# Optimization experiments

Hardware: AMD Instinct MI355X
Metric: run time of the kernel (lower is better)

## Reference

```python
import jax, jax.numpy as jnp
import numpy as np

NUM_LAYERS = 4
HIDDEN = 32
INPUT = 2
B = 16384
T = 64


def setup_inputs() -> dict:
    key = jax.random.key(0)
    ks = jax.random.split(key, 8)
    s = 1.0 / np.sqrt(HIDDEN)  # PyTorch LSTM default init scale
    return {
        "x": jax.random.normal(ks[0], (B, 3, T), dtype=jnp.float32),
        "W_ih0": jax.random.uniform(ks[1], (4 * HIDDEN, INPUT), minval=-s, maxval=s, dtype=jnp.float32),
        "W_ih": jax.random.uniform(ks[2], (NUM_LAYERS - 1, 4 * HIDDEN, HIDDEN), minval=-s, maxval=s, dtype=jnp.float32),
        "W_hh": jax.random.uniform(ks[3], (NUM_LAYERS, 4 * HIDDEN, HIDDEN), minval=-s, maxval=s, dtype=jnp.float32),
        "b_ih": jax.random.uniform(ks[4], (NUM_LAYERS, 4 * HIDDEN), minval=-s, maxval=s, dtype=jnp.float32),
        "b_hh": jax.random.uniform(ks[5], (NUM_LAYERS, 4 * HIDDEN), minval=-s, maxval=s, dtype=jnp.float32),
        "W_lin": jax.random.uniform(ks[6], (1, HIDDEN), minval=-s, maxval=s, dtype=jnp.float32),
        "b_lin": jax.random.uniform(ks[7], (1,), minval=-s, maxval=s, dtype=jnp.float32),
    }


def _lstm_cell(inp, h, c, Wih, Whh, b):
    # inp: [B, in_dim]; h, c: [B, H]; Wih: [4H, in_dim]; Whh: [4H, H]; b: [4H]
    gates = inp @ Wih.T + h @ Whh.T + b  # [B, 4H]
    i, f, g, o = jnp.split(gates, 4, axis=-1)  # PyTorch gate order: i, f, g, o
    i = jax.nn.sigmoid(i)
    f = jax.nn.sigmoid(f)
    g = jnp.tanh(g)
    o = jax.nn.sigmoid(o)
    c_new = f * c + i * g
    h_new = o * jnp.tanh(c_new)
    return h_new, c_new


def reference(x, W_ih0, W_ih, W_hh, b_ih, b_hh, W_lin, b_lin):
    # x: [B, 3, T]; channel 2 (id) is discarded, as in the original forward.
    feats = x[:, :2, :]                         # [B, 2, T]
    xs = jnp.transpose(feats, (2, 0, 1))        # [T, B, 2]
    bsz = x.shape[0]
    h0 = jnp.zeros((NUM_LAYERS, bsz, HIDDEN), dtype=x.dtype)
    c0 = jnp.zeros((NUM_LAYERS, bsz, HIDDEN), dtype=x.dtype)
    bias = b_ih + b_hh  # [L, 4H]

    def step(carry, xt):
        h, c = carry  # each [L, B, H]
        inp = xt
        hs, cs = [], []
        for l in range(NUM_LAYERS):
            Wih = W_ih0 if l == 0 else W_ih[l - 1]
            h_new, c_new = _lstm_cell(inp, h[l], c[l], Wih, W_hh[l], bias[l])
            hs.append(h_new)
            cs.append(c_new)
            inp = h_new
        return (jnp.stack(hs), jnp.stack(cs)), None

    (h, c), _ = jax.lax.scan(step, (h0, c0), xs)
    # last timestep's top-layer output -> linear -> sigmoid -> squeeze to [B]
    out = jax.nn.sigmoid(h[-1] @ W_lin.T + b_lin)  # [B, 1]
    return out.squeeze(-1)
```

## Files before the change

kernel.cpp:

```cpp
#include <hip/hip_runtime.h>

typedef float  f32x4  __attribute__((ext_vector_type(4)));
typedef float  f32x2  __attribute__((ext_vector_type(2)));
typedef short  bf16x8 __attribute__((ext_vector_type(8)));

#define TWOLOG2E   2.8853900817779268f
#define NLOG2E    -1.4426950408889634f
#define NTWOLOG2E -2.8853900817779268f

__device__ __forceinline__ unsigned short f2b(float f) {
    unsigned int u = __builtin_bit_cast(unsigned int, f);
    u += 0x7fffu + ((u >> 16) & 1u);
    return (unsigned short)(u >> 16);
}
__device__ __forceinline__ float b2f(unsigned short s) {
    unsigned int u = ((unsigned int)s) << 16;
    return __builtin_bit_cast(float, u);
}
__device__ __forceinline__ unsigned int pk2(float lo, float hi) {
#if __has_builtin(__builtin_amdgcn_cvt_pk_bf16_f32)
    typedef __bf16 bf16x2 __attribute__((ext_vector_type(2)));
    bf16x2 p = __builtin_amdgcn_cvt_pk_bf16_f32(lo, hi);
    return __builtin_bit_cast(unsigned int, p);
#else
    return (unsigned int)f2b(lo) | ((unsigned int)f2b(hi) << 16);
#endif
}
__device__ __forceinline__ float frcp(float x) { return __builtin_amdgcn_rcpf(x); }
__device__ __forceinline__ float fex2(float x) { return __builtin_amdgcn_exp2f(x); }

__global__ __launch_bounds__(256, 2)
void lstm_mfma(const float* __restrict__ xg,  const float* __restrict__ Wih0,
               const float* __restrict__ Wih, const float* __restrict__ Whh,
               const float* __restrict__ bih, const float* __restrict__ bhh,
               const float* __restrict__ Wlin,const float* __restrict__ blin,
               float* __restrict__ out) {
    __shared__ short        hb[16 * 1280] __attribute__((aligned(16)));
    __shared__ unsigned int xb[64 * 32];

    const int tid  = threadIdx.x;
    const int wv   = __builtin_amdgcn_readfirstlane(tid >> 6);
    const int lane = tid & 63;
    const int m    = lane & 15;
    const int q    = lane >> 4;
    const int row0 = blockIdx.x * 32;

    for (int i = tid; i < 10240; i += 256) ((unsigned int*)hb)[i] = 0u;

    for (int i = tid; i < 2048; i += 256) {
        int r = i >> 6, t = i & 63;
        float x0 = xg[(size_t)(row0 + r) * 192 + t];
        float x1 = xg[(size_t)(row0 + r) * 192 + 64 + t];
        xb[t * 32 + r] = pk2(x0, x1);
    }

    bf16x8 bfr[8][2];
    float  bv[8];
#pragma unroll
    for (int g = 0; g < 8; ++g) {
        const int   T    = g >> 1;
        const int   rowG = T * 32 + 2 * m + (g & 1);
        const float sc   = (T == 2) ? NTWOLOG2E : NLOG2E;
        bv[g] = (bih[wv * 128 + rowG] + bhh[wv * 128 + rowG]) * sc;
#pragma unroll
        for (int c = 0; c < 2; ++c) {
            const int k0 = c * 32 + q * 8;
            float w[8];
            if (wv == 0) {
                if (c == 0) {
#pragma unroll
                    for (int jj = 0; jj < 8; ++jj) w[jj] = 0.0f;
                    if (q == 0) { w[0] = Wih0[rowG * 2]; w[1] = Wih0[rowG * 2 + 1]; }
                } else {
                    const float* src = Whh + rowG * 32 + (k0 - 32);
#pragma unroll
                    for (int jj = 0; jj < 8; ++jj) w[jj] = src[jj];
                }
            } else {
                const float* src = (c == 0) ? (Wih + (wv - 1) * 4096 + rowG * 32 + k0)
                                            : (Whh + wv * 4096 + rowG * 32 + (k0 - 32));
#pragma unroll
                for (int jj = 0; jj < 8; ++jj) w[jj] = src[jj];
            }
            bf16x8 fr;
#pragma unroll
            for (int jj = 0; jj < 8; ++jj) fr[jj] = (short)f2b(w[jj] * sc);
            bfr[g][c] = fr;
        }
    }

    f32x4 cbq[8];
#pragma unroll
    for (int g = 0; g < 8; ++g) {
        f32x4 c4 = {bv[g], bv[g], bv[g], bv[g]};
        cbq[g] = c4;
    }

    f32x2 cp2[2][4];
#pragma unroll
    for (int tt = 0; tt < 2; ++tt)
#pragma unroll
        for (int r = 0; r < 4; ++r) cp2[tt][r] = (f32x2){0.0f, 0.0f};

    const int aoff = m * 40 + q * 8;
    const int woff = q * 80 + m;

    __syncthreads();

    auto cell_step = [&](int t, const short* pa0, const short* pa1, short* hwr) {
        bf16x8 a0[2], a1[2];
#pragma unroll
        for (int tt = 0; tt < 2; ++tt) {
            if (wv == 0) {
                unsigned int xd = xb[t * 32 + tt * 16 + m];
                union { unsigned int u[4]; bf16x8 v; } au;
                au.u[0] = (q == 0) ? xd : 0u; au.u[1] = 0u; au.u[2] = 0u; au.u[3] = 0u;
                a0[tt] = au.v;
            } else {
                a0[tt] = *(const bf16x8*)(pa0 + aoff + tt * 640);
            }
            a1[tt] = *(const bf16x8*)(pa1 + aoff + tt * 640);
        }
#pragma unroll
        for (int tt = 0; tt < 2; ++tt) {
            f32x4 acc[8];
#pragma unroll
            for (int g = 0; g < 8; ++g) {
                acc[g] = __builtin_amdgcn_mfma_f32_16x16x32_bf16(a0[tt], bfr[g][0], cbq[g], 0, 0, 0);
                acc[g] = __builtin_amdgcn_mfma_f32_16x16x32_bf16(a1[tt], bfr[g][1], acc[g], 0, 0, 0);
            }
            const f32x2 one  = {1.0f, 1.0f};
            const f32x2 c2l  = {TWOLOG2E, TWOLOG2E};
            const f32x2 n2l  = {NTWOLOG2E, NTWOLOG2E};
#pragma unroll
            for (int r = 0; r < 4; ++r) {
                f32x2 ei = {fex2(acc[0][r]), fex2(acc[1][r])};
                f32x2 ef = {fex2(acc[2][r]), fex2(acc[3][r])};
                f32x2 eg = {fex2(acc[4][r]), fex2(acc[5][r])};
                f32x2 eo = {fex2(acc[6][r]), fex2(acc[7][r])};
                f32x2 apf = one + ef;
                f32x2 p1  = (one + ei) * (one + eg);
                f32x2 Dc  = p1 * apf;
                f32x2 R_  = {frcp(Dc.x), frcp(Dc.y)};
                f32x2 egp = __builtin_elementwise_fma(eg, c2l, n2l);
                f32x2 t1  = egp * apf;
                f32x2 t2  = __builtin_elementwise_fma(cp2[tt][r], p1, t1);
                f32x2 cn  = t2 * R_;
                cp2[tt][r] = cn;
                f32x2 ec  = {fex2(cn.x), fex2(cn.y)};
                f32x2 Dh  = (one + eo) * (one + ec);
                f32x2 Rh  = {frcp(Dh.x), frcp(Dh.y)};
                f32x2 hh  = (one - ec) * Rh;
                ((unsigned int*)hwr)[woff + tt * 320 + r * 20] = pk2(hh.x, hh.y);
            }
        }
    };

    for (int S = 0; S < 35; ++S) {
        const int t0 = 2 * (S - wv);
        if (t0 >= 0 && t0 <= 62) {
            const int p  = S & 1;
            const int pb = p ^ 1;
            short*       Lc0 = hb + ((wv * 2 + p ) * 2    ) * 1280;
            short*       Lc1 = Lc0 + 1280;
            const short* Lp1 = hb + ((wv * 2 + pb) * 2 + 1) * 1280;
            const int    lb  = (wv > 0) ? (wv - 1) : 0;
            const short* Dp0 = hb + ((lb * 2 + pb) * 2    ) * 1280;
            const short* Dp1 = Dp0 + 1280;

            cell_step(t0,     Dp0, Lp1, Lc0);
            cell_step(t0 + 1, Dp1, Lc0, Lc1);
        }
        __syncthreads();
    }

    if (tid < 32) {
        const short* h3 = hb + ((3 * 2 + 0) * 2 + 1) * 1280;
        float s = blin[0];
#pragma unroll
        for (int k = 0; k < 32; ++k)
            s += Wlin[k] * b2f((unsigned short)h3[tid * 40 + k]);
        out[row0 + tid] = frcp(1.0f + fex2(s * NLOG2E));
    }
}

extern "C" void kernel_launch(void* const* d_in, const int* in_sizes, int n_in,
                              void* d_out, int out_size, void* d_ws, size_t ws_size,
                              hipStream_t stream) {
    const float* x    = (const float*)d_in[0];
    const float* Wih0 = (const float*)d_in[1];
    const float* Wih  = (const float*)d_in[2];
    const float* Whh  = (const float*)d_in[3];
    const float* bih  = (const float*)d_in[4];
    const float* bhh  = (const float*)d_in[5];
    const float* Wlin = (const float*)d_in[6];
    const float* blin = (const float*)d_in[7];
    float* out = (float*)d_out;

    lstm_mfma<<<512, 256, 0, stream>>>(x, Wih0, Wih, Whh, bih, bhh, Wlin, blin, out);
}
```

Measured before the change: 215.5 us.

## Halve rows per block to 16 and raise occupancy to four blocks per CU

Each block now handles 16 batch rows instead of 32, so the grid doubles to 1024 blocks and shared memory per block halves. The launch bound goes from 2 to 4 blocks per CU, and the bias is added after the MFMA instead of being held in a replicated accumulator, which cuts register use. The aim is more concurrent waves to hide the latency of the serial recurrence chain. In exchange, each wave gets less independent MFMA work per step, since two 16-row tiles no longer interleave.

```diff
diff --git a/kernel.cpp b/kernel.cpp
--- a/kernel.cpp
+++ b/kernel.cpp
@@ -29,29 +29,29 @@
 __device__ __forceinline__ float frcp(float x) { return __builtin_amdgcn_rcpf(x); }
 __device__ __forceinline__ float fex2(float x) { return __builtin_amdgcn_exp2f(x); }
 
-__global__ __launch_bounds__(256, 2)
+__global__ __launch_bounds__(256, 4)
 void lstm_mfma(const float* __restrict__ xg,  const float* __restrict__ Wih0,
                const float* __restrict__ Wih, const float* __restrict__ Whh,
                const float* __restrict__ bih, const float* __restrict__ bhh,
                const float* __restrict__ Wlin,const float* __restrict__ blin,
                float* __restrict__ out) {
-    __shared__ short        hb[16 * 1280] __attribute__((aligned(16)));
-    __shared__ unsigned int xb[64 * 32];
+    __shared__ short        hb[16 * 640] __attribute__((aligned(16)));
+    __shared__ unsigned int xb[64 * 16];
 
     const int tid  = threadIdx.x;
     const int wv   = __builtin_amdgcn_readfirstlane(tid >> 6);
     const int lane = tid & 63;
     const int m    = lane & 15;
     const int q    = lane >> 4;
-    const int row0 = blockIdx.x * 32;
+    const int row0 = blockIdx.x * 16;
 
-    for (int i = tid; i < 10240; i += 256) ((unsigned int*)hb)[i] = 0u;
+    for (int i = tid; i < 5120; i += 256) ((unsigned int*)hb)[i] = 0u;
 
-    for (int i = tid; i < 2048; i += 256) {
+    for (int i = tid; i < 1024; i += 256) {
         int r = i >> 6, t = i & 63;
         float x0 = xg[(size_t)(row0 + r) * 192 + t];
         float x1 = xg[(size_t)(row0 + r) * 192 + 64 + t];
-        xb[t * 32 + r] = pk2(x0, x1);
+        xb[t * 16 + r] = pk2(x0, x1);
     }
 
     bf16x8 bfr[8][2];
@@ -89,18 +89,13 @@
         }
     }
 
-    f32x4 cbq[8];
+    f32x2 bvp[4];
 #pragma unroll
-    for (int g = 0; g < 8; ++g) {
-        f32x4 c4 = {bv[g], bv[g], bv[g], bv[g]};
-        cbq[g] = c4;
-    }
+    for (int T = 0; T < 4; ++T) bvp[T] = (f32x2){bv[2 * T], bv[2 * T + 1]};
 
-    f32x2 cp2[2][4];
+    f32x2 cp2[4];
 #pragma unroll
-    for (int tt = 0; tt < 2; ++tt)
-#pragma unroll
-        for (int r = 0; r < 4; ++r) cp2[tt][r] = (f32x2){0.0f, 0.0f};
+    for (int r = 0; r < 4; ++r) cp2[r] = (f32x2){0.0f, 0.0f};
 
     const int aoff = m * 40 + q * 8;
     const int woff = q * 80 + m;
@@ -108,51 +103,51 @@
     __syncthreads();
 
     auto cell_step = [&](int t, const short* pa0, const short* pa1, short* hwr) {
-        bf16x8 a0[2], a1[2];
+        bf16x8 a0, a1;
+        if (wv == 0) {
+            unsigned int xd = xb[t * 16 + m];
+            union { unsigned int u[4]; bf16x8 v; } au;
+            au.u[0] = (q == 0) ? xd : 0u; au.u[1] = 0u; au.u[2] = 0u; au.u[3] = 0u;
+            a0 = au.v;
+        } else {
+            a0 = *(const bf16x8*)(pa0 + aoff);
+        }
+        a1 = *(const bf16x8*)(pa1 + aoff);
+
+        const f32x4 zq = {0.0f, 0.0f, 0.0f, 0.0f};
+        f32x4 acc[8];
 #pragma unroll
-        for (int tt = 0; tt < 2; ++tt) {
-            if (wv == 0) {
-                unsigned int xd = xb[t * 32 + tt * 16 + m];
-                union { unsigned int u[4]; bf16x8 v; } au;
-                au.u[0] = (q == 0) ? xd : 0u; au.u[1] = 0u; au.u[2] = 0u; au.u[3] = 0u;
-                a0[tt] = au.v;
-            } else {
-                a0[tt] = *(const bf16x8*)(pa0 + aoff + tt * 640);
-            }
-            a1[tt] = *(const bf16x8*)(pa1 + aoff + tt * 640);
+        for (int g = 0; g < 8; ++g) {
+            acc[g] = __builtin_amdgcn_mfma_f32_16x16x32_bf16(a0, bfr[g][0], zq, 0, 0, 0);
+            acc[g] = __builtin_amdgcn_mfma_f32_16x16x32_bf16(a1, bfr[g][1], acc[g], 0, 0, 0);
         }
+        const f32x2 one  = {1.0f, 1.0f};
+        const f32x2 c2l  = {TWOLOG2E, TWOLOG2E};
+        const f32x2 n2l  = {NTWOLOG2E, NTWOLOG2E};
 #pragma unroll
-        for (int tt = 0; tt < 2; ++tt) {
-            f32x4 acc[8];
-#pragma unroll
-            for (int g = 0; g < 8; ++g) {
-                acc[g] = __builtin_amdgcn_mfma_f32_16x16x32_bf16(a0[tt], bfr[g][0], cbq[g], 0, 0, 0);
-                acc[g] = __builtin_amdgcn_mfma_f32_16x16x32_bf16(a1[tt], bfr[g][1], acc[g], 0, 0, 0);
-            }
-            const f32x2 one  = {1.0f, 1.0f};
-            const f32x2 c2l  = {TWOLOG2E, TWOLOG2E};
-            const f32x2 n2l  = {NTWOLOG2E, NTWOLOG2E};
-#pragma unroll
-            for (int r = 0; r < 4; ++r) {
-                f32x2 ei = {fex2(acc[0][r]), fex2(acc[1][r])};
-                f32x2 ef = {fex2(acc[2][r]), fex2(acc[3][r])};
-                f32x2 eg = {fex2(acc[4][r]), fex2(acc[5][r])};
-                f32x2 eo = {fex2(acc[6][r]), fex2(acc[7][r])};
-                f32x2 apf = one + ef;
-                f32x2 p1  = (one + ei) * (one + eg);
-                f32x2 Dc  = p1 * apf;
-                f32x2 R_  = {frcp(Dc.x), frcp(Dc.y)};
-                f32x2 egp = __builtin_elementwise_fma(eg, c2l, n2l);
-                f32x2 t1  = egp * apf;
-                f32x2 t2  = __builtin_elementwise_fma(cp2[tt][r], p1, t1);
-                f32x2 cn  = t2 * R_;
-                cp2[tt][r] = cn;
-                f32x2 ec  = {fex2(cn.x), fex2(cn.y)};
-                f32x2 Dh  = (one + eo) * (one + ec);
-                f32x2 Rh  = {frcp(Dh.x), frcp(Dh.y)};
-                f32x2 hh  = (one - ec) * Rh;
-                ((unsigned int*)hwr)[woff + tt * 320 + r * 20] = pk2(hh.x, hh.y);
-            }
+        for (int r = 0; r < 4; ++r) {
+            f32x2 gi = (f32x2){acc[0][r], acc[1][r]} + bvp[0];
+            f32x2 gf = (f32x2){acc[2][r], acc[3][r]} + bvp[1];
+            f32x2 gg = (f32x2){acc[4][r], acc[5][r]} + bvp[2];
+            f32x2 go = (f32x2){acc[6][r], acc[7][r]} + bvp[3];
+            f32x2 ei = {fex2(gi.x), fex2(gi.y)};
+            f32x2 ef = {fex2(gf.x), fex2(gf.y)};
+            f32x2 eg = {fex2(gg.x), fex2(gg.y)};
+            f32x2 eo = {fex2(go.x), fex2(go.y)};
+            f32x2 apf = one + ef;
+            f32x2 p1  = (one + ei) * (one + eg);
+            f32x2 Dc  = p1 * apf;
+            f32x2 R_  = {frcp(Dc.x), frcp(Dc.y)};
+            f32x2 egp = __builtin_elementwise_fma(eg, c2l, n2l);
+            f32x2 t1  = egp * apf;
+            f32x2 t2  = __builtin_elementwise_fma(cp2[r], p1, t1);
+            f32x2 cn  = t2 * R_;
+            cp2[r] = cn;
+            f32x2 ec  = {fex2(cn.x), fex2(cn.y)};
+            f32x2 Dh  = (one + eo) * (one + ec);
+            f32x2 Rh  = {frcp(Dh.x), frcp(Dh.y)};
+            f32x2 hh  = (one - ec) * Rh;
+            ((unsigned int*)hwr)[woff + r * 20] = pk2(hh.x, hh.y);
         }
     };
 
@@ -161,12 +156,12 @@
         if (t0 >= 0 && t0 <= 62) {
             const int p  = S & 1;
             const int pb = p ^ 1;
-            short*       Lc0 = hb + ((wv * 2 + p ) * 2    ) * 1280;
-            short*       Lc1 = Lc0 + 1280;
-            const short* Lp1 = hb + ((wv * 2 + pb) * 2 + 1) * 1280;
+            short*       Lc0 = hb + ((wv * 2 + p ) * 2    ) * 640;
+            short*       Lc1 = Lc0 + 640;
+            const short* Lp1 = hb + ((wv * 2 + pb) * 2 + 1) * 640;
             const int    lb  = (wv > 0) ? (wv - 1) : 0;
-            const short* Dp0 = hb + ((lb * 2 + pb) * 2    ) * 1280;
-            const short* Dp1 = Dp0 + 1280;
+            const short* Dp0 = hb + ((lb * 2 + pb) * 2    ) * 640;
+            const short* Dp1 = Dp0 + 640;
 
             cell_step(t0,     Dp0, Lp1, Lc0);
             cell_step(t0 + 1, Dp1, Lc0, Lc1);
@@ -174,8 +169,8 @@
         __syncthreads();
     }
 
-    if (tid < 32) {
-        const short* h3 = hb + ((3 * 2 + 0) * 2 + 1) * 1280;
+    if (tid < 16) {
+        const short* h3 = hb + ((3 * 2 + 0) * 2 + 1) * 640;
         float s = blin[0];
 #pragma unroll
         for (int k = 0; k < 32; ++k)
@@ -197,5 +192,5 @@
     const float* blin = (const float*)d_in[7];
     float* out = (float*)d_out;
 
-    lstm_mfma<<<512, 256, 0, stream>>>(x, Wih0, Wih, Whh, bih, bhh, Wlin, blin, out);
+    lstm_mfma<<<1024, 256, 0, stream>>>(x, Wih0, Wih, Whh, bih, bhh, Wlin, blin, out);
 }
```

Measured after the change: 245.4 us. +13.9%, slower.

## Interleave next-timestep input MFMAs with current-step epilogue in LSTM wavefront

Applied to the files above, without the earlier changes.

Splits each two-timestep cell update into separate input-projection and recurrent MFMA phases. The input-side MFMAs for the second timestep are issued between the epilogue tiles of the first timestep, so matrix work overlaps with the exp/rcp epilogue. The bias moves from the MFMA accumulator init into the epilogue as a vector add. This roughly doubles the live accumulator registers, which risks spills or reduced occupancy.

```diff
diff --git a/kernel.cpp b/kernel.cpp
--- a/kernel.cpp
+++ b/kernel.cpp
@@ -89,12 +89,9 @@
         }
     }
 
-    f32x4 cbq[8];
-#pragma unroll
-    for (int g = 0; g < 8; ++g) {
-        f32x4 c4 = {bv[g], bv[g], bv[g], bv[g]};
-        cbq[g] = c4;
-    }
+    f32x2 bvp[4];
+#pragma unroll
+    for (int T = 0; T < 4; ++T) bvp[T] = (f32x2){bv[2 * T], bv[2 * T + 1]};
 
     f32x2 cp2[2][4];
 #pragma unroll
@@ -107,54 +104,59 @@
 
     __syncthreads();
 
-    auto cell_step = [&](int t, const short* pa0, const short* pa1, short* hwr) {
-        bf16x8 a0[2], a1[2];
-#pragma unroll
-        for (int tt = 0; tt < 2; ++tt) {
-            if (wv == 0) {
+    auto load_down = [&](int t, const short* pa, bf16x8* dst) {
+        if (wv == 0) {
+#pragma unroll
+            for (int tt = 0; tt < 2; ++tt) {
                 unsigned int xd = xb[t * 32 + tt * 16 + m];
                 union { unsigned int u[4]; bf16x8 v; } au;
                 au.u[0] = (q == 0) ? xd : 0u; au.u[1] = 0u; au.u[2] = 0u; au.u[3] = 0u;
-                a0[tt] = au.v;
-            } else {
-                a0[tt] = *(const bf16x8*)(pa0 + aoff + tt * 640);
+                dst[tt] = au.v;
             }
-            a1[tt] = *(const bf16x8*)(pa1 + aoff + tt * 640);
-        }
-#pragma unroll
-        for (int tt = 0; tt < 2; ++tt) {
-            f32x4 acc[8];
-#pragma unroll
-            for (int g = 0; g < 8; ++g) {
-                acc[g] = __builtin_amdgcn_mfma_f32_16x16x32_bf16(a0[tt], bfr[g][0], cbq[g], 0, 0, 0);
-                acc[g] = __builtin_amdgcn_mfma_f32_16x16x32_bf16(a1[tt], bfr[g][1], acc[g], 0, 0, 0);
-            }
-            const f32x2 one  = {1.0f, 1.0f};
-            const f32x2 c2l  = {TWOLOG2E, TWOLOG2E};
-            const f32x2 n2l  = {NTWOLOG2E, NTWOLOG2E};
-#pragma unroll
-            for (int r = 0; r < 4; ++r) {
-                f32x2 ei = {fex2(acc[0][r]), fex2(acc[1][r])};
-                f32x2 ef = {fex2(acc[2][r]), fex2(acc[3][r])};
-                f32x2 eg = {fex2(acc[4][r]), fex2(acc[5][r])};
-                f32x2 eo = {fex2(acc[6][r]), fex2(acc[7][r])};
-                f32x2 apf = one + ef;
-                f32x2 p1  = (one + ei) * (one + eg);
-                f32x2 Dc  = p1 * apf;
-                f32x2 R_  = {frcp(Dc.x), frcp(Dc.y)};
-                f32x2 egp = __builtin_elementwise_fma(eg, c2l, n2l);
-                f32x2 t1  = egp * apf;
-                f32x2 t2  = __builtin_elementwise_fma(cp2[tt][r], p1, t1);
-                f32x2 cn  = t2 * R_;
-                cp2[tt][r] = cn;
-                f32x2 ec  = {fex2(cn.x), fex2(cn.y)};
-                f32x2 Dh  = (one + eo) * (one + ec);
-                f32x2 Rh  = {frcp(Dh.x), frcp(Dh.y)};
-                f32x2 hh  = (one - ec) * Rh;
-                ((unsigned int*)hwr)[woff + tt * 320 + r * 20] = pk2(hh.x, hh.y);
-            }
+        } else {
+#pragma unroll
+            for (int tt = 0; tt < 2; ++tt)
+                dst[tt] = *(const bf16x8*)(pa + aoff + tt * 640);
         }
     };
+    auto load_rec = [&](const short* pa, bf16x8* dst) {
+#pragma unroll
+        for (int tt = 0; tt < 2; ++tt)
+            dst[tt] = *(const bf16x8*)(pa + aoff + tt * 640);
+    };
+
+    auto epi_tile = [&](const f32x4* a8, f32x2* cpr, short* hwr, int tt) {
+        const f32x2 one = {1.0f, 1.0f};
+        const f32x2 c2l = {TWOLOG2E, TWOLOG2E};
+        const f32x2 n2l = {NTWOLOG2E, NTWOLOG2E};
+#pragma unroll
+        for (int r = 0; r < 4; ++r) {
+            f32x2 gi = (f32x2){a8[0][r], a8[1][r]} + bvp[0];
+            f32x2 gf = (f32x2){a8[2][r], a8[3][r]} + bvp[1];
+            f32x2 gg = (f32x2){a8[4][r], a8[5][r]} + bvp[2];
+            f32x2 go = (f32x2){a8[6][r], a8[7][r]} + bvp[3];
+            f32x2 ei = {fex2(gi.x), fex2(gi.y)};
+            f32x2 ef = {fex2(gf.x), fex2(gf.y)};
+            f32x2 eg = {fex2(gg.x), fex2(gg.y)};
+            f32x2 eo = {fex2(go.x), fex2(go.y)};
+            f32x2 apf = one + ef;
+            f32x2 p1  = (one + ei) * (one + eg);
+            f32x2 Dc  = p1 * apf;
+            f32x2 R_  = {frcp(Dc.x), frcp(Dc.y)};
+            f32x2 egp = __builtin_elementwise_fma(eg, c2l, n2l);
+            f32x2 t1  = egp * apf;
+            f32x2 t2  = __builtin_elementwise_fma(cpr[r], p1, t1);
+            f32x2 cn  = t2 * R_;
+            cpr[r] = cn;
+            f32x2 ec  = {fex2(cn.x), fex2(cn.y)};
+            f32x2 Dh  = (one + eo) * (one + ec);
+            f32x2 Rh  = {frcp(Dh.x), frcp(Dh.y)};
+            f32x2 hh  = (one - ec) * Rh;
+            ((unsigned int*)hwr)[woff + tt * 320 + r * 20] = pk2(hh.x, hh.y);
+        }
+    };
+
+    const f32x4 zq = {0.0f, 0.0f, 0.0f, 0.0f};
 
     for (int S = 0; S < 35; ++S) {
         const int t0 = 2 * (S - wv);
@@ -168,8 +170,37 @@
             const short* Dp0 = hb + ((lb * 2 + pb) * 2    ) * 1280;
             const short* Dp1 = Dp0 + 1280;
 
-            cell_step(t0,     Dp0, Lp1, Lc0);
-            cell_step(t0 + 1, Dp1, Lc0, Lc1);
+            bf16x8 a0d[2], a0r[2], a1d[2];
+            load_down(t0,     Dp0, a0d);
+            load_rec (Lp1,         a0r);
+            load_down(t0 + 1, Dp1, a1d);
+
+            f32x4 acc0[2][8], acc1[2][8];
+#pragma unroll
+            for (int tt = 0; tt < 2; ++tt)
+#pragma unroll
+                for (int g = 0; g < 8; ++g) {
+                    acc0[tt][g] = __builtin_amdgcn_mfma_f32_16x16x32_bf16(a0d[tt], bfr[g][0], zq, 0, 0, 0);
+                    acc0[tt][g] = __builtin_amdgcn_mfma_f32_16x16x32_bf16(a0r[tt], bfr[g][1], acc0[tt][g], 0, 0, 0);
+                }
+
+            epi_tile(acc0[0], cp2[0], Lc0, 0);
+#pragma unroll
+            for (int tt = 0; tt < 2; ++tt)
+#pragma unroll
+                for (int g = 0; g < 8; ++g)
+                    acc1[tt][g] = __builtin_amdgcn_mfma_f32_16x16x32_bf16(a1d[tt], bfr[g][0], zq, 0, 0, 0);
+            epi_tile(acc0[1], cp2[1], Lc0, 1);
+
+            bf16x8 a1r[2];
+            load_rec(Lc0, a1r);
+#pragma unroll
+            for (int tt = 0; tt < 2; ++tt)
+#pragma unroll
+                for (int g = 0; g < 8; ++g)
+                    acc1[tt][g] = __builtin_amdgcn_mfma_f32_16x16x32_bf16(a1r[tt], bfr[g][1], acc1[tt][g], 0, 0, 0);
+            epi_tile(acc1[0], cp2[0], Lc1, 0);
+            epi_tile(acc1[1], cp2[1], Lc1, 1);
         }
         __syncthreads();
     }
```

New measurement: 231.6 us. +7.5%, slower.

## Transpose MFMA operands so LSTM hidden state stays in registers

Applied to the files above, without the earlier changes.

Swaps the MFMA operand roles so the weights become the A operand and the hidden state becomes the B operand, with gate rows permuted so that each lane's accumulator outputs line up directly with the next step's B-operand layout. The recurrent hidden state is kept in registers (hreg) rather than re-read from LDS, and LDS writes become one 16-byte vector store per lane instead of scattered 4-byte stores. This removes the same-layer LDS read and the LDS zero-init, at the cost of more involved index permutations for weights, biases and the final linear readout.

```diff
diff --git a/kernel.cpp b/kernel.cpp
--- a/kernel.cpp
+++ b/kernel.cpp
@@ -35,7 +35,7 @@
                const float* __restrict__ bih, const float* __restrict__ bhh,
                const float* __restrict__ Wlin,const float* __restrict__ blin,
                float* __restrict__ out) {
-    __shared__ short        hb[16 * 1280] __attribute__((aligned(16)));
+    __shared__ unsigned int hb[16 * 512] __attribute__((aligned(16)));
     __shared__ unsigned int xb[64 * 32];
 
     const int tid  = threadIdx.x;
@@ -45,8 +45,6 @@
     const int q    = lane >> 4;
     const int row0 = blockIdx.x * 32;
 
-    for (int i = tid; i < 10240; i += 256) ((unsigned int*)hb)[i] = 0u;
-
     for (int i = tid; i < 2048; i += 256) {
         int r = i >> 6, t = i & 63;
         float x0 = xg[(size_t)(row0 + r) * 192 + t];
@@ -54,105 +52,116 @@
         xb[t * 32 + r] = pk2(x0, x1);
     }
 
-    bf16x8 bfr[8][2];
-    float  bv[8];
+    bf16x8 afr[2][8];
+    f32x4  cbq[8];
 #pragma unroll
     for (int g = 0; g < 8; ++g) {
-        const int   T    = g >> 1;
-        const int   rowG = T * 32 + 2 * m + (g & 1);
-        const float sc   = (T == 2) ? NTWOLOG2E : NLOG2E;
-        bv[g] = (bih[wv * 128 + rowG] + bhh[wv * 128 + rowG]) * sc;
-#pragma unroll
-        for (int c = 0; c < 2; ++c) {
-            const int k0 = c * 32 + q * 8;
+        const int   u_m  = 8 * (m >> 2) + 2 * (g & 3) + (m & 1);
+        const int   gt_m = 2 * (g >> 2) + ((m >> 1) & 1);
+        const int   rowG = gt_m * 32 + u_m;
+        const float sc   = (gt_m == 2) ? NTWOLOG2E : NLOG2E;
+        {
             float w[8];
             if (wv == 0) {
-                if (c == 0) {
-#pragma unroll
-                    for (int jj = 0; jj < 8; ++jj) w[jj] = 0.0f;
-                    if (q == 0) { w[0] = Wih0[rowG * 2]; w[1] = Wih0[rowG * 2 + 1]; }
-                } else {
-                    const float* src = Whh + rowG * 32 + (k0 - 32);
-#pragma unroll
-                    for (int jj = 0; jj < 8; ++jj) w[jj] = src[jj];
-                }
+#pragma unroll
+                for (int jj = 0; jj < 8; ++jj) w[jj] = 0.0f;
+                if (q == 0) { w[0] = Wih0[rowG * 2]; w[1] = Wih0[rowG * 2 + 1]; }
             } else {
-                const float* src = (c == 0) ? (Wih + (wv - 1) * 4096 + rowG * 32 + k0)
-                                            : (Whh + wv * 4096 + rowG * 32 + (k0 - 32));
+                const float* src = Wih + (wv - 1) * 4096 + rowG * 32 + q * 8;
 #pragma unroll
                 for (int jj = 0; jj < 8; ++jj) w[jj] = src[jj];
             }
             bf16x8 fr;
 #pragma unroll
             for (int jj = 0; jj < 8; ++jj) fr[jj] = (short)f2b(w[jj] * sc);
-            bfr[g][c] = fr;
-        }
-    }
-
-    f32x4 cbq[8];
-#pragma unroll
-    for (int g = 0; g < 8; ++g) {
-        f32x4 c4 = {bv[g], bv[g], bv[g], bv[g]};
+            afr[0][g] = fr;
+        }
+        {
+            const float* src = Whh + wv * 4096 + rowG * 32 + q * 8;
+            bf16x8 fr;
+#pragma unroll
+            for (int jj = 0; jj < 8; ++jj) fr[jj] = (short)f2b(src[jj] * sc);
+            afr[1][g] = fr;
+        }
+        f32x4 c4;
+#pragma unroll
+        for (int r = 0; r < 4; ++r) {
+            const int   u_r  = 8 * q + 2 * (g & 3) + (r & 1);
+            const int   gt_r = 2 * (g >> 2) + ((r >> 1) & 1);
+            const float scr  = (gt_r == 2) ? NTWOLOG2E : NLOG2E;
+            c4[r] = (bih[wv * 128 + gt_r * 32 + u_r] + bhh[wv * 128 + gt_r * 32 + u_r]) * scr;
+        }
         cbq[g] = c4;
     }
 
+    bf16x8 hreg[2];
+#pragma unroll
+    for (int tt = 0; tt < 2; ++tt) {
+        union { unsigned int u[4]; bf16x8 v; } z;
+        z.u[0] = 0u; z.u[1] = 0u; z.u[2] = 0u; z.u[3] = 0u;
+        hreg[tt] = z.v;
+    }
     f32x2 cp2[2][4];
 #pragma unroll
     for (int tt = 0; tt < 2; ++tt)
 #pragma unroll
-        for (int r = 0; r < 4; ++r) cp2[tt][r] = (f32x2){0.0f, 0.0f};
-
-    const int aoff = m * 40 + q * 8;
-    const int woff = q * 80 + m;
+        for (int j = 0; j < 4; ++j) cp2[tt][j] = (f32x2){0.0f, 0.0f};
 
     __syncthreads();
 
-    auto cell_step = [&](int t, const short* pa0, const short* pa1, short* hwr) {
-        bf16x8 a0[2], a1[2];
+    auto chain = [&](f32x2 ai, f32x2 af, f32x2 ag, f32x2 ao, f32x2& cpr) -> f32x2 {
+        const f32x2 one = {1.0f, 1.0f};
+        const f32x2 c2l = {TWOLOG2E, TWOLOG2E};
+        const f32x2 n2l = {NTWOLOG2E, NTWOLOG2E};
+        f32x2 ei = {fex2(ai.x), fex2(ai.y)};
+        f32x2 ef = {fex2(af.x), fex2(af.y)};
+        f32x2 eg = {fex2(ag.x), fex2(ag.y)};
+        f32x2 eo = {fex2(ao.x), fex2(ao.y)};
+        f32x2 apf = one + ef;
+        f32x2 p1  = (one + ei) * (one + eg);
+        f32x2 Dc  = p1 * apf;
+        f32x2 R_  = {frcp(Dc.x), frcp(Dc.y)};
+        f32x2 egp = __builtin_elementwise_fma(eg, c2l, n2l);
+        f32x2 t1  = egp * apf;
+        f32x2 t2  = __builtin_elementwise_fma(cpr, p1, t1);
+        f32x2 cn  = t2 * R_;
+        cpr = cn;
+        f32x2 ec  = {fex2(cn.x), fex2(cn.y)};
+        f32x2 Dh  = (one + eo) * (one + ec);
+        f32x2 Rh  = {frcp(Dh.x), frcp(Dh.y)};
+        return (one - ec) * Rh;
+    };
+
+    auto cell_step = [&](int t, const unsigned int* pin, unsigned int* pout) {
 #pragma unroll
         for (int tt = 0; tt < 2; ++tt) {
+            bf16x8 bin;
             if (wv == 0) {
                 unsigned int xd = xb[t * 32 + tt * 16 + m];
                 union { unsigned int u[4]; bf16x8 v; } au;
                 au.u[0] = (q == 0) ? xd : 0u; au.u[1] = 0u; au.u[2] = 0u; au.u[3] = 0u;
-                a0[tt] = au.v;
+                bin = au.v;
             } else {
-                a0[tt] = *(const bf16x8*)(pa0 + aoff + tt * 640);
-            }
-            a1[tt] = *(const bf16x8*)(pa1 + aoff + tt * 640);
-        }
-#pragma unroll
-        for (int tt = 0; tt < 2; ++tt) {
+                bin = *(const bf16x8*)(pin + tt * 256 + lane * 4);
+            }
             f32x4 acc[8];
 #pragma unroll
             for (int g = 0; g < 8; ++g) {
-                acc[g] = __builtin_amdgcn_mfma_f32_16x16x32_bf16(a0[tt], bfr[g][0], cbq[g], 0, 0, 0);
-                acc[g] = __builtin_amdgcn_mfma_f32_16x16x32_bf16(a1[tt], bfr[g][1], acc[g], 0, 0, 0);
-            }
-            const f32x2 one  = {1.0f, 1.0f};
-            const f32x2 c2l  = {TWOLOG2E, TWOLOG2E};
-            const f32x2 n2l  = {NTWOLOG2E, NTWOLOG2E};
-#pragma unroll
-            for (int r = 0; r < 4; ++r) {
-                f32x2 ei = {fex2(acc[0][r]), fex2(acc[1][r])};
-                f32x2 ef = {fex2(acc[2][r]), fex2(acc[3][r])};
-                f32x2 eg = {fex2(acc[4][r]), fex2(acc[5][r])};
-                f32x2 eo = {fex2(acc[6][r]), fex2(acc[7][r])};
-                f32x2 apf = one + ef;
-                f32x2 p1  = (one + ei) * (one + eg);
-                f32x2 Dc  = p1 * apf;
-                f32x2 R_  = {frcp(Dc.x), frcp(Dc.y)};
-                f32x2 egp = __builtin_elementwise_fma(eg, c2l, n2l);
-                f32x2 t1  = egp * apf;
-                f32x2 t2  = __builtin_elementwise_fma(cp2[tt][r], p1, t1);
-                f32x2 cn  = t2 * R_;
-                cp2[tt][r] = cn;
-                f32x2 ec  = {fex2(cn.x), fex2(cn.y)};
-                f32x2 Dh  = (one + eo) * (one + ec);
-                f32x2 Rh  = {frcp(Dh.x), frcp(Dh.y)};
-                f32x2 hh  = (one - ec) * Rh;
-                ((unsigned int*)hwr)[woff + tt * 320 + r * 20] = pk2(hh.x, hh.y);
-            }
+                acc[g] = __builtin_amdgcn_mfma_f32_16x16x32_bf16(afr[0][g], bin, cbq[g], 0, 0, 0);
+                acc[g] = __builtin_amdgcn_mfma_f32_16x16x32_bf16(afr[1][g], hreg[tt], acc[g], 0, 0, 0);
+            }
+            union { unsigned int u[4]; bf16x8 v; } hn;
+#pragma unroll
+            for (int j = 0; j < 4; ++j) {
+                f32x2 ai = (f32x2)__builtin_shufflevector(acc[j],     acc[j],     0, 1);
+                f32x2 af = (f32x2)__builtin_shufflevector(acc[j],     acc[j],     2, 3);
+                f32x2 ag = (f32x2)__builtin_shufflevector(acc[4 + j], acc[4 + j], 0, 1);
+                f32x2 ao = (f32x2)__builtin_shufflevector(acc[4 + j], acc[4 + j], 2, 3);
+                f32x2 hh = chain(ai, af, ag, ao, cp2[tt][j]);
+                hn.u[j] = pk2(hh.x, hh.y);
+            }
+            hreg[tt] = hn.v;
+            *(bf16x8*)(pout + tt * 256 + lane * 4) = hn.v;
         }
     };
 
@@ -161,25 +170,31 @@
         if (t0 >= 0 && t0 <= 62) {
             const int p  = S & 1;
             const int pb = p ^ 1;
-            short*       Lc0 = hb + ((wv * 2 + p ) * 2    ) * 1280;
-            short*       Lc1 = Lc0 + 1280;
-            const short* Lp1 = hb + ((wv * 2 + pb) * 2 + 1) * 1280;
-            const int    lb  = (wv > 0) ? (wv - 1) : 0;
-            const short* Dp0 = hb + ((lb * 2 + pb) * 2    ) * 1280;
-            const short* Dp1 = Dp0 + 1280;
-
-            cell_step(t0,     Dp0, Lp1, Lc0);
-            cell_step(t0 + 1, Dp1, Lc0, Lc1);
+            unsigned int*       Lc0 = hb + ((wv * 2 + p ) * 2    ) * 512;
+            unsigned int*       Lc1 = Lc0 + 512;
+            const int           lb  = (wv > 0) ? (wv - 1) : 0;
+            const unsigned int* Dp0 = hb + ((lb * 2 + pb) * 2    ) * 512;
+            const unsigned int* Dp1 = Dp0 + 512;
+
+            cell_step(t0,     Dp0, Lc0);
+            cell_step(t0 + 1, Dp1, Lc1);
         }
         __syncthreads();
     }
 
     if (tid < 32) {
-        const short* h3 = hb + ((3 * 2 + 0) * 2 + 1) * 1280;
+        const unsigned int* h3 = hb + ((3 * 2 + 0) * 2 + 1) * 512;
+        const int tt = tid >> 4, mm = tid & 15;
         float s = blin[0];
 #pragma unroll
-        for (int k = 0; k < 32; ++k)
-            s += Wlin[k] * b2f((unsigned short)h3[tid * 40 + k]);
+        for (int qq = 0; qq < 4; ++qq)
+#pragma unroll
+            for (int j = 0; j < 4; ++j) {
+                unsigned int w2 = h3[tt * 256 + (qq * 16 + mm) * 4 + j];
+                const int u0 = 8 * qq + 2 * j;
+                s += Wlin[u0]     * b2f((unsigned short)(w2 & 0xffffu));
+                s += Wlin[u0 + 1] * b2f((unsigned short)(w2 >> 16));
+            }
         out[row0 + tid] = frcp(1.0f + fex2(s * NLOG2E));
     }
 }
```

Result: slower. 220.4 us (+2.3%).
